# Kernel tuning notes

Measured on AMD Instinct MI355X. Metric: run time of the kernel, lower is better.

The kernel has to match this reference:

```python
import jax, jax.numpy as jnp
import numpy as np

N, NF, DIM, H, DH, DEPTH, EDIM, NB = 256, 127, 128, 8, 64, 6, 3, 512
INNER = H * DH  # 512
SCALE = DH ** -0.5
EPS = 1e-5


def setup_inputs() -> dict:
    key = jax.random.key(0)
    ks = jax.random.split(key, 16)
    p = lambda k, shape: jax.random.normal(k, shape, jnp.float32) * 0.02
    return {
        "coordinates": jax.random.normal(ks[0], (N, 3), jnp.float32),
        "bonds": jax.random.randint(ks[1], (NB, 2), 0, N),
        "noise_level": jax.random.uniform(ks[2], (1,), jnp.float32),
        "atom_emb": p(ks[3], (N, NF)),
        "ln1_g": jnp.ones((DEPTH, DIM)), "ln1_b": jnp.zeros((DEPTH, DIM)),
        "Wq": p(ks[4], (DEPTH, DIM, INNER)), "bq": jnp.zeros((DEPTH, INNER)),
        "Wkv": p(ks[5], (DEPTH, DIM, 2 * INNER)), "bkv": jnp.zeros((DEPTH, 2 * INNER)),
        "We": p(ks[6], (DEPTH, EDIM, INNER)), "be": jnp.zeros((DEPTH, INNER)),
        "Wo": p(ks[7], (DEPTH, INNER, DIM)), "bo": jnp.zeros((DEPTH, DIM)),
        "Wg1": p(ks[8], (DEPTH, 3 * DIM)),
        "ln2_g": jnp.ones((DEPTH, DIM)), "ln2_b": jnp.zeros((DEPTH, DIM)),
        "W1": p(ks[9], (DEPTH, DIM, 4 * DIM)), "b1": jnp.zeros((DEPTH, 4 * DIM)),
        "W2": p(ks[10], (DEPTH, 4 * DIM, DIM)), "b2": jnp.zeros((DEPTH, DIM)),
        "Wg2": p(ks[11], (DEPTH, 3 * DIM)),
        "out_w": p(ks[12], (DIM, 1)), "out_b": jnp.zeros((1,)),
    }


def _layernorm(x, g, b):
    m = jnp.mean(x, axis=-1, keepdims=True)
    v = jnp.mean((x - m) ** 2, axis=-1, keepdims=True)
    return (x - m) * jax.lax.rsqrt(v + EPS) * g + b


def _gated_residual(x, res, Wg):
    # Linear(3*dim -> 1, no bias) then sigmoid; mask is all-True so no masking.
    gate = jax.nn.sigmoid(jnp.concatenate([x, res, x - res], axis=-1) @ Wg)[..., None]
    return x * gate + res * (1.0 - gate)


def _forward(coordinates, bonds, noise_level, atom_emb, ln1_g, ln1_b, Wq, bq,
             Wkv, bkv, We, be, Wo, bo, Wg1, ln2_g, ln2_b, W1, b1, W2, b2, Wg2,
             out_w, out_b):
    n = coordinates.shape[0]
    # nodes: [n, NF] atom embeddings (looked up at arange(n)) + noise column -> [n, DIM]
    noise_col = jnp.broadcast_to(noise_level.reshape(1, 1), (n, 1))
    nodes = jnp.concatenate([atom_emb, noise_col], axis=-1)
    # dense edge tensor [n, n, 3]: coordinate differences at bonded pairs, antisymmetric
    bi, bj = bonds[:, 0], bonds[:, 1]
    diff = coordinates[bi] - coordinates[bj]
    edges = jnp.zeros((n, n, EDIM), jnp.float32).at[bi, bj].set(diff).at[bj, bi].set(-diff)

    for l in range(DEPTH):
        # --- edge-biased multi-head attention (PreNorm) ---
        x = _layernorm(nodes, ln1_g[l], ln1_b[l])
        q = (x @ Wq[l] + bq[l]).reshape(n, H, DH).transpose(1, 0, 2)          # [h, i, d]
        kv = x @ Wkv[l] + bkv[l]
        k = kv[:, :INNER].reshape(n, H, DH).transpose(1, 0, 2)                # [h, j, d]
        v = kv[:, INNER:].reshape(n, H, DH).transpose(1, 0, 2)                # [h, j, d]
        e = (edges @ We[l] + be[l]).reshape(n, n, H, DH).transpose(2, 0, 1, 3)  # [h, i, j, d]
        k_ij = k[:, None, :, :] + e                                            # [h, i, j, d]
        v_ij = v[:, None, :, :] + e
        sim = jnp.einsum('hid,hijd->hij', q, k_ij) * SCALE
        attn = jax.nn.softmax(sim, axis=-1)  # mask is all ones -> no-op
        out = jnp.einsum('hij,hijd->hid', attn, v_ij)                          # [h, i, d]
        out = out.transpose(1, 0, 2).reshape(n, INNER) @ Wo[l] + bo[l]         # [n, DIM]
        nodes = _gated_residual(out, nodes, Wg1[l])
        # --- feedforward (PreNorm) + gated residual ---
        y = _layernorm(nodes, ln2_g[l], ln2_b[l])
        y = jax.nn.gelu(y @ W1[l] + b1[l], approximate=False) @ W2[l] + b2[l]
        nodes = _gated_residual(y, nodes, Wg2[l])

    energy = nodes @ out_w + out_b  # [n, 1]
    return energy[None, :, :]       # [1, n, 1]


def reference(coordinates, bonds, noise_level, atom_emb, ln1_g, ln1_b, Wq, bq,
              Wkv, bkv, We, be, Wo, bo, Wg1, ln2_g, ln2_b, W1, b1, W2, b2, Wg2,
              out_w, out_b):
    return _forward(coordinates, bonds, noise_level, atom_emb, ln1_g, ln1_b,
                    Wq, bq, Wkv, bkv, We, be, Wo, bo, Wg1, ln2_g, ln2_b,
                    W1, b1, W2, b2, Wg2, out_w, out_b)
```

## Files before the change

### kernel.cpp

```cpp
#include <hip/hip_runtime.h>

#define NN     256
#define NF     127
#define DIM    128
#define NH     8
#define DH     64
#define INNER  512
#define DEPTH  6
#define NB     512
#define ATTN_SCALE 0.125f
#define LN_EPS 1e-5f

#define FMA4(A_, S_, V_) { A_.x=fmaf(S_,(V_).x,A_.x); A_.y=fmaf(S_,(V_).y,A_.y); \
                           A_.z=fmaf(S_,(V_).z,A_.z); A_.w=fmaf(S_,(V_).w,A_.w); }

__device__ __forceinline__ float wred_sum(float v){
#pragma unroll
  for(int o=32;o;o>>=1) v += __shfl_xor(v,o);
  return v;
}
__device__ __forceinline__ float wred_max(float v){
#pragma unroll
  for(int o=32;o;o>>=1) v = fmaxf(v,__shfl_xor(v,o));
  return v;
}
__device__ __forceinline__ float2 wred_sum2(float a, float b){
#pragma unroll
  for(int o=32;o;o>>=1){ a += __shfl_xor(a,o); b += __shfl_xor(b,o); }
  return make_float2(a,b);
}

__device__ __forceinline__ void ln_wave(float n0, float n1,
                                        const float* g, const float* b, int l,
                                        float& x0, float& x1){
  float2 sv = wred_sum2(n0+n1, n0*n0+n1*n1);
  float m  = sv.x*(1.f/DIM);
  float var = sv.y*(1.f/DIM) - m*m;
  float rs = rsqrtf(var + LN_EPS);
  x0 = (n0-m)*rs*g[l]    + b[l];
  x1 = (n1-m)*rs*g[64+l] + b[64+l];
}

__device__ __forceinline__ void gate_wave(float o0, float o1, float& n0, float& n1,
                                          const float* Wg, int l){
  float gv = o0*Wg[l]    + n0*Wg[DIM+l]    + (o0-n0)*Wg[2*DIM+l]
           + o1*Wg[64+l] + n1*Wg[DIM+64+l] + (o1-n1)*Wg[2*DIM+64+l];
  gv = wred_sum(gv);
  float gate = 1.f/(1.f + expf(-gv));
  n0 = o0*gate + n0*(1.f-gate);
  n1 = o1*gate + n1*(1.f-gate);
}

__device__ __forceinline__ void mvp128_512(const float* xin, const float* W,
                                           float* SC, int t){
  const int cg4 = (t&127)<<2, fq = t>>7;
  float4 acc = make_float4(0.f,0.f,0.f,0.f);
#pragma unroll 8
  for(int f=fq*32; f<fq*32+32; f++){
    float4 wv = *(const float4*)(W + f*INNER + cg4);
    float xv = xin[f];
    FMA4(acc, xv, wv);
  }
  *(float4*)(SC + fq*INNER + cg4) = acc;
}
__device__ __forceinline__ void mvp128_1024(const float* xin, const float* W,
                                            float* SC, int t){
  const int cg4 = (t&255)<<2, rh = t>>8;
  float4 acc = make_float4(0.f,0.f,0.f,0.f);
#pragma unroll 8
  for(int f=rh*64; f<rh*64+64; f++){
    float4 wv = *(const float4*)(W + f*(2*INNER) + cg4);
    float xv = xin[f];
    FMA4(acc, xv, wv);
  }
  *(float4*)(SC + rh*(2*INNER) + cg4) = acc;
}
__device__ __forceinline__ void mvp512_128(const float* ain, const float* W,
                                           float* SC, int t){
  const int cg4 = (t&31)<<2, fg = t>>5;
  float4 acc = make_float4(0.f,0.f,0.f,0.f);
#pragma unroll 8
  for(int f=fg*32; f<fg*32+32; f++){
    float4 wv = *(const float4*)(W + f*DIM + cg4);
    float av = ain[f];
    FMA4(acc, av, wv);
  }
  *(float4*)(SC + fg*DIM + cg4) = acc;
}

__device__ __forceinline__ void qkv_tail(const float* xs, int i,
    const float* Wq, const float* bq, const float* Wkv, const float* bkv,
    const float* be, float* qgn, float* kTn, float* vgn, float* SC, int t){
  mvp128_512(xs, Wq, SC, t);
  __syncthreads();
  qgn[i*INNER + t] = bq[t] + SC[t] + SC[INNER+t] + SC[2*INNER+t] + SC[3*INNER+t];
  __syncthreads();
  mvp128_1024(xs, Wkv, SC, t);
  __syncthreads();
#pragma unroll
  for(int cc=0; cc<2; cc++){
    int c = t + cc*512;
    float s = bkv[c] + SC[c] + SC[2*INNER+c];
    if(c < INNER) kTn[c*NN + i]            = s + be[c];
    else          vgn[i*INNER + c - INNER] = s + be[c-INNER];
  }
}

__global__ __launch_bounds__(512) void k_qkv0(const float* atom_emb, const float* noise,
    float* nodes, const float* ln1_g, const float* ln1_b,
    const float* Wq, const float* bq, const float* Wkv, const float* bkv, const float* be,
    float* qg, float* kT, float* vg,
    const int* bonds, const float* coords, float* ebg){
  __shared__ __align__(16) float SC[2048];
  __shared__ __align__(16) float xsm[DIM];
  __shared__ __align__(16) float ebs[8*768];
  const int t = threadIdx.x, bid = blockIdx.x;
  if(bid >= NN){
    const int i0 = (bid-NN)<<3;
#pragma unroll
    for(int cc=0; cc<12; cc++) ebs[cc*512 + t] = 0.f;
    __syncthreads();
    {
      const int bi = bonds[2*t], bj = bonds[2*t+1];
      const bool hi = (bi>=i0 && bi<i0+8), hj = (bj>=i0 && bj<i0+8);
      if(hi || hj){
        float dx = coords[3*bi+0] - coords[3*bj+0];
        float dy = coords[3*bi+1] - coords[3*bj+1];
        float dz = coords[3*bi+2] - coords[3*bj+2];
        if(hi){ float* e = ebs + (bi-i0)*768; e[bj]=dx;  e[256+bj]=dy;  e[512+bj]=dz;  }
        if(hj){ float* e = ebs + (bj-i0)*768; e[bi]=-dx; e[256+bi]=-dy; e[512+bi]=-dz; }
      }
    }
    __syncthreads();
#pragma unroll
    for(int cc=0; cc<12; cc++) ebg[(size_t)i0*768 + cc*512 + t] = ebs[cc*512 + t];
    return;
  }
  const int i = bid, w = t>>6, l = t&63;
  float nd0 = (l<NF)?    atom_emb[i*NF + l]      : noise[0];
  float nd1 = (64+l<NF)? atom_emb[i*NF + 64 + l] : noise[0];
  if(w==0){ nodes[i*DIM + l] = nd0; nodes[i*DIM + 64 + l] = nd1; }
  float x0, x1;
  ln_wave(nd0, nd1, ln1_g, ln1_b, l, x0, x1);
  xsm[l] = x0; xsm[64+l] = x1;
  __syncthreads();
  qkv_tail(xsm, i, Wq, bq, Wkv, bkv, be, qg, kT, vg, SC, t);
}

__global__ __launch_bounds__(512) void k_attn(
    const float* __restrict__ qg, const float* __restrict__ kT,
    const float* __restrict__ vg, const float* __restrict__ ebg,
    const float* __restrict__ We, float* __restrict__ aog,
    const float* __restrict__ pfA, const float* __restrict__ pfB,
    const float* __restrict__ pfC, const float* __restrict__ pfD,
    const float* __restrict__ pfE, int pf_next)
{
  __shared__ __align__(16) float qsm[8*DH];
  __shared__ __align__(16) float aW[8][NN];
  const int t = threadIdx.x;
  const int h = blockIdx.x >> 5, i0 = (blockIdx.x & 31) << 3;
  const int w = t>>6, l = t&63;
  const int qb = h*DH, j0 = l<<2;

  qsm[w*DH + l] = qg[(i0+w)*INNER + qb + l];

  {
    const int s = blockIdx.x >> 3;
    float keep = 0.f;
    { float4 v = ((const float4*)pfA)[s*512 + t];  keep += v.x+v.y+v.z+v.w; }
    { float4 v = ((const float4*)pfB)[s*512 + t];  keep += v.x+v.y+v.z+v.w; }
    { float4 v = ((const float4*)pfC)[s*512 + t];  keep += v.x+v.y+v.z+v.w; }
    if(pf_next){
      { float4 v = ((const float4*)pfD)[s*512 + t];        keep += v.x+v.y+v.z+v.w; }
      { float4 v = ((const float4*)pfE)[s*1024 + t];       keep += v.x+v.y+v.z+v.w; }
      { float4 v = ((const float4*)pfE)[s*1024 + 512 + t]; keep += v.x+v.y+v.z+v.w; }
    }
    asm volatile("" :: "v"(keep));
  }
  __syncthreads();

  float qwe0, qwe1, qwe2;
  {
    float qv = qsm[w*DH + l];
    qwe0 = qv*We[0*INNER + qb + l];
    qwe1 = qv*We[1*INNER + qb + l];
    qwe2 = qv*We[2*INNER + qb + l];
#pragma unroll
    for(int o=32;o;o>>=1){
      qwe0 += __shfl_xor(qwe0,o); qwe1 += __shfl_xor(qwe1,o); qwe2 += __shfl_xor(qwe2,o);
    }
  }
  const float* __restrict__ kTh = kT + qb*NN;
  float s0=0.f,s1=0.f,s2=0.f,s3=0.f;
#pragma unroll 8
  for(int o=0;o<DH;o++){
    float qv = qsm[w*DH + o];
    float4 kk = *(const float4*)(kTh + o*NN + j0);
    s0=fmaf(qv,kk.x,s0); s1=fmaf(qv,kk.y,s1); s2=fmaf(qv,kk.z,s2); s3=fmaf(qv,kk.w,s3);
  }
  const float* __restrict__ e = ebg + (size_t)(i0+w)*768;
  float4 ex = *(const float4*)(e + j0);
  float4 ey = *(const float4*)(e + 256 + j0);
  float4 ez = *(const float4*)(e + 512 + j0);
  s0 = (s0 + qwe0*ex.x + qwe1*ey.x + qwe2*ez.x)*ATTN_SCALE;
  s1 = (s1 + qwe0*ex.y + qwe1*ey.y + qwe2*ez.y)*ATTN_SCALE;
  s2 = (s2 + qwe0*ex.z + qwe1*ey.z + qwe2*ez.z)*ATTN_SCALE;
  s3 = (s3 + qwe0*ex.w + qwe1*ey.w + qwe2*ez.w)*ATTN_SCALE;
  float mx = wred_max(fmaxf(fmaxf(s0,s1),fmaxf(s2,s3)));
  float p0=expf(s0-mx), p1=expf(s1-mx), p2=expf(s2-mx), p3=expf(s3-mx);
  float inv = 1.f / wred_sum(p0+p1+p2+p3);
  float a0=p0*inv, a1=p1*inv, a2=p2*inv, a3=p3*inv;
  *(float4*)(aW[w] + j0) = make_float4(a0,a1,a2,a3);
  float c0 = a0*ex.x + a1*ex.y + a2*ex.z + a3*ex.w;
  float c1 = a0*ey.x + a1*ey.y + a2*ey.z + a3*ey.w;
  float c2 = a0*ez.x + a1*ez.y + a2*ez.z + a3*ez.w;
  c0 = wred_sum(c0); c1 = wred_sum(c1); c2 = wred_sum(c2);
  __builtin_amdgcn_wave_barrier();
  const int dq = (l&15)<<2, jg = l>>4;
  const float* __restrict__ vb = vg + qb + dq;
  float4 acc = make_float4(0.f,0.f,0.f,0.f);
#pragma unroll 8
  for(int jj=0;jj<64;jj++){
    int j = (jg<<6) + ((jj + (jg<<3)) & 63);
    float a = aW[w][j];
    float4 vv = *(const float4*)(vb + j*INNER);
    FMA4(acc, a, vv);
  }
#pragma unroll
  for(int o=16;o<64;o<<=1){
    acc.x += __shfl_xor(acc.x,o); acc.y += __shfl_xor(acc.y,o);
    acc.z += __shfl_xor(acc.z,o); acc.w += __shfl_xor(acc.w,o);
  }
  if(l<16){
    float4 we0 = *(const float4*)(We + 0*INNER + qb + dq);
    float4 we1 = *(const float4*)(We + 1*INNER + qb + dq);
    float4 we2 = *(const float4*)(We + 2*INNER + qb + dq);
    float4 ov;
    ov.x = acc.x + c0*we0.x + c1*we1.x + c2*we2.x;
    ov.y = acc.y + c0*we0.y + c1*we1.y + c2*we2.y;
    ov.z = acc.z + c0*we0.z + c1*we1.z + c2*we2.z;
    ov.w = acc.w + c0*we0.w + c1*we1.w + c2*we2.w;
    *(float4*)(aog + (i0+w)*INNER + qb + dq) = ov;
  }
}

__global__ __launch_bounds__(512) void k_layer(
    float* nodes, const float* __restrict__ aog,
    float* qg_n, float* kT_n, float* vg_n,
    const float* __restrict__ Wo, const float* __restrict__ bo,
    const float* __restrict__ Wg1,
    const float* __restrict__ ln2_g, const float* __restrict__ ln2_b,
    const float* __restrict__ W1, const float* __restrict__ b1,
    const float* __restrict__ W2, const float* __restrict__ b2,
    const float* __restrict__ Wg2,
    const float* __restrict__ ln1_g_n, const float* __restrict__ ln1_b_n,
    const float* __restrict__ Wq_n, const float* __restrict__ bq_n,
    const float* __restrict__ Wkv_n, const float* __restrict__ bkv_n,
    const float* __restrict__ be_n,
    const float* __restrict__ out_w, const float* __restrict__ out_b,
    float* eout, int has_next)
{
  __shared__ __align__(16) float SC[2048];
  __shared__ __align__(16) float qs[INNER];
  __shared__ __align__(16) float aos[INNER];
  __shared__ __align__(16) float xsm[DIM];
  const int t = threadIdx.x, i = blockIdx.x;
  const int w = t>>6, l = t&63;

  aos[t] = aog[i*INNER + t];
  float nd0 = nodes[i*DIM + l];
  float nd1 = nodes[i*DIM + 64 + l];
  __syncthreads();

  mvp512_128(aos, Wo, SC, t);
  __syncthreads();
  {
    float o0 = bo[l], o1 = bo[64+l];
#pragma unroll
    for(int fg=0; fg<16; fg++){ o0 += SC[fg*DIM + l]; o1 += SC[fg*DIM + 64 + l]; }
    gate_wave(o0, o1, nd0, nd1, Wg1, l);
    float x0, x1;
    ln_wave(nd0, nd1, ln2_g, ln2_b, l, x0, x1);
    xsm[l] = x0; xsm[64+l] = x1;
  }
  __syncthreads();

  mvp128_512(xsm, W1, SC, t);
  __syncthreads();
  {
    float a = b1[t] + SC[t] + SC[INNER+t] + SC[2*INNER+t] + SC[3*INNER+t];
    qs[t] = 0.5f*a*(1.f + erff(a*0.70710678118654752440f));
  }
  __syncthreads();
  mvp512_128(qs, W2, SC, t);
  __syncthreads();
  {
    float y0 = b2[l], y1 = b2[64+l];
#pragma unroll
    for(int fg=0; fg<16; fg++){ y0 += SC[fg*DIM + l]; y1 += SC[fg*DIM + 64 + l]; }
    gate_wave(y0, y1, nd0, nd1, Wg2, l);
    if(w==0){ nodes[i*DIM + l] = nd0; nodes[i*DIM + 64 + l] = nd1; }
    if(has_next){
      float x0, x1;
      ln_wave(nd0, nd1, ln1_g_n, ln1_b_n, l, x0, x1);
      xsm[l] = x0; xsm[64+l] = x1;
    } else if(w==0){
      float ev = nd0*out_w[l] + nd1*out_w[64+l];
      ev = wred_sum(ev);
      if(l==0) eout[i] = ev + out_b[0];
    }
  }
  if(has_next){
    __syncthreads();
    qkv_tail(xsm, i, Wq_n, bq_n, Wkv_n, bkv_n, be_n,
             qg_n, kT_n, vg_n, SC, t);
  }
}

extern "C" void kernel_launch(void* const* d_in, const int* in_sizes, int n_in,
                              void* d_out, int out_size, void* d_ws, size_t ws_size,
                              hipStream_t stream){
  const float* coords   = (const float*)d_in[0];
  const int*   bonds    = (const int*  )d_in[1];
  const float* noise    = (const float*)d_in[2];
  const float* atom_emb = (const float*)d_in[3];
  const float* ln1_g = (const float*)d_in[4];
  const float* ln1_b = (const float*)d_in[5];
  const float* Wq    = (const float*)d_in[6];
  const float* bq    = (const float*)d_in[7];
  const float* Wkv   = (const float*)d_in[8];
  const float* bkv   = (const float*)d_in[9];
  const float* We    = (const float*)d_in[10];
  const float* be    = (const float*)d_in[11];
  const float* Wo    = (const float*)d_in[12];
  const float* bo    = (const float*)d_in[13];
  const float* Wg1   = (const float*)d_in[14];
  const float* ln2_g = (const float*)d_in[15];
  const float* ln2_b = (const float*)d_in[16];
  const float* W1    = (const float*)d_in[17];
  const float* b1    = (const float*)d_in[18];
  const float* W2    = (const float*)d_in[19];
  const float* b2    = (const float*)d_in[20];
  const float* Wg2   = (const float*)d_in[21];
  const float* out_w = (const float*)d_in[22];
  const float* out_b = (const float*)d_in[23];

  float* ws = (float*)d_ws;
  float* nodes   = ws;
  float* qbuf[2] = { ws +  32768, ws + 163840 };
  float* kbuf[2] = { ws + 294912, ws + 425984 };
  float* vbuf[2] = { ws + 557056, ws + 688128 };
  float* aobuf   = ws + 819200;
  float* ebg     = ws + 950272;

  k_qkv0<<<NN+32, 512, 0, stream>>>(atom_emb, noise, nodes, ln1_g, ln1_b,
                                    Wq, bq, Wkv, bkv, be,
                                    qbuf[0], kbuf[0], vbuf[0],
                                    bonds, coords, ebg);
  for(int l=0; l<DEPTH; l++){
    int cur = l&1, nxt = cur^1;
    int has_next = (l < DEPTH-1);
    int ln = has_next ? l+1 : l;
    const float* Wo_l = Wo + (size_t)l*INNER*DIM;
    const float* W1_l = W1 + (size_t)l*DIM*4*DIM;
    const float* W2_l = W2 + (size_t)l*4*DIM*DIM;
    const float* Wq_n = Wq  + (size_t)ln*DIM*INNER;
    const float* Wkv_n= Wkv + (size_t)ln*DIM*2*INNER;
    k_attn<<<NN, 512, 0, stream>>>(
      qbuf[cur], kbuf[cur], vbuf[cur], ebg,
      We + (size_t)l*3*INNER, aobuf,
      Wo_l, W1_l, W2_l, Wq_n, Wkv_n, has_next);
    k_layer<<<NN, 512, 0, stream>>>(
      nodes, aobuf,
      qbuf[nxt], kbuf[nxt], vbuf[nxt],
      Wo_l, bo + (size_t)l*DIM, Wg1 + (size_t)l*3*DIM,
      ln2_g + (size_t)l*DIM, ln2_b + (size_t)l*DIM,
      W1_l, b1 + (size_t)l*4*DIM,
      W2_l, b2 + (size_t)l*DIM, Wg2 + (size_t)l*3*DIM,
      ln1_g + (size_t)ln*DIM, ln1_b + (size_t)ln*DIM,
      Wq_n, bq + (size_t)ln*INNER,
      Wkv_n, bkv + (size_t)ln*2*INNER,
      be  + (size_t)ln*INNER,
      out_w, out_b, (float*)d_out, has_next);
  }
}
```

Before: 296.3 us.

## Convert Wq/Wo/W1/W2 weights to fp16 and overlap Q with KV matvec

Adds a prep kernel that converts the Wq, Wo, W1 and W2 weights to fp16 once per call. The per-node matrix-vector products then read half as many weight bytes, using 8-wide loads that accumulate in fp32. The L2 prefetch in the attention kernel is resized to match the fp16 layout. In qkv_tail, the Q and KV products now run back to back into separate shared-memory regions with a single barrier, which needs a larger shared buffer and adds an extra kernel launch plus fp16 rounding error in those weights.

```diff
diff --git a/kernel.cpp b/kernel.cpp
--- a/kernel.cpp
+++ b/kernel.cpp
@@ -11,6 +11,9 @@
 #define ATTN_SCALE 0.125f
 #define LN_EPS 1e-5f
 
+typedef _Float16 f16;
+union H8 { uint4 u; f16 h[8]; };
+
 #define FMA4(A_, S_, V_) { A_.x=fmaf(S_,(V_).x,A_.x); A_.y=fmaf(S_,(V_).y,A_.y); \
                            A_.z=fmaf(S_,(V_).z,A_.z); A_.w=fmaf(S_,(V_).w,A_.w); }
 
@@ -51,20 +54,45 @@
   n1 = o1*gate + n1*(1.f-gate);
 }
 
-__device__ __forceinline__ void mvp128_512(const float* xin, const float* W,
-                                           float* SC, int t){
-  const int cg4 = (t&127)<<2, fq = t>>7;
-  float4 acc = make_float4(0.f,0.f,0.f,0.f);
-#pragma unroll 8
-  for(int f=fq*32; f<fq*32+32; f++){
-    float4 wv = *(const float4*)(W + f*INNER + cg4);
-    float xv = xin[f];
-    FMA4(acc, xv, wv);
-  }
-  *(float4*)(SC + fq*INNER + cg4) = acc;
-}
-__device__ __forceinline__ void mvp128_1024(const float* xin, const float* W,
-                                            float* SC, int t){
+__device__ __forceinline__ void mvp128_512h(const float* __restrict__ xin,
+                                            const f16* __restrict__ W,
+                                            float* __restrict__ SC, int t){
+  const int cg8 = (t&63)<<3, fg = t>>6, f0 = fg<<4;
+  const f16* __restrict__ p = W + f0*INNER + cg8;
+  float4 a0 = make_float4(0.f,0.f,0.f,0.f), a1 = a0;
+#pragma unroll
+  for(int k=0;k<16;k++){
+    H8 wv; wv.u = *(const uint4*)(p + k*INNER);
+    float x = xin[f0+k];
+    a0.x=fmaf(x,(float)wv.h[0],a0.x); a0.y=fmaf(x,(float)wv.h[1],a0.y);
+    a0.z=fmaf(x,(float)wv.h[2],a0.z); a0.w=fmaf(x,(float)wv.h[3],a0.w);
+    a1.x=fmaf(x,(float)wv.h[4],a1.x); a1.y=fmaf(x,(float)wv.h[5],a1.y);
+    a1.z=fmaf(x,(float)wv.h[6],a1.z); a1.w=fmaf(x,(float)wv.h[7],a1.w);
+  }
+  *(float4*)(SC + fg*INNER + cg8)     = a0;
+  *(float4*)(SC + fg*INNER + cg8 + 4) = a1;
+}
+__device__ __forceinline__ void mvp512_128h(const float* __restrict__ ain,
+                                            const f16* __restrict__ W,
+                                            float* __restrict__ SC, int t){
+  const int cg8 = (t&15)<<3, fg = t>>4, f0 = fg<<4;
+  const f16* __restrict__ p = W + f0*DIM + cg8;
+  float4 a0 = make_float4(0.f,0.f,0.f,0.f), a1 = a0;
+#pragma unroll
+  for(int k=0;k<16;k++){
+    H8 wv; wv.u = *(const uint4*)(p + k*DIM);
+    float x = ain[f0+k];
+    a0.x=fmaf(x,(float)wv.h[0],a0.x); a0.y=fmaf(x,(float)wv.h[1],a0.y);
+    a0.z=fmaf(x,(float)wv.h[2],a0.z); a0.w=fmaf(x,(float)wv.h[3],a0.w);
+    a1.x=fmaf(x,(float)wv.h[4],a1.x); a1.y=fmaf(x,(float)wv.h[5],a1.y);
+    a1.z=fmaf(x,(float)wv.h[6],a1.z); a1.w=fmaf(x,(float)wv.h[7],a1.w);
+  }
+  *(float4*)(SC + fg*DIM + cg8)     = a0;
+  *(float4*)(SC + fg*DIM + cg8 + 4) = a1;
+}
+__device__ __forceinline__ void mvp128_1024(const float* __restrict__ xin,
+                                            const float* __restrict__ W,
+                                            float* __restrict__ SC, int t){
   const int cg4 = (t&255)<<2, rh = t>>8;
   float4 acc = make_float4(0.f,0.f,0.f,0.f);
 #pragma unroll 8
@@ -75,43 +103,53 @@
   }
   *(float4*)(SC + rh*(2*INNER) + cg4) = acc;
 }
-__device__ __forceinline__ void mvp512_128(const float* ain, const float* W,
-                                           float* SC, int t){
-  const int cg4 = (t&31)<<2, fg = t>>5;
-  float4 acc = make_float4(0.f,0.f,0.f,0.f);
-#pragma unroll 8
-  for(int f=fg*32; f<fg*32+32; f++){
-    float4 wv = *(const float4*)(W + f*DIM + cg4);
-    float av = ain[f];
-    FMA4(acc, av, wv);
-  }
-  *(float4*)(SC + fg*DIM + cg4) = acc;
-}
-
-__device__ __forceinline__ void qkv_tail(const float* xs, int i,
-    const float* Wq, const float* bq, const float* Wkv, const float* bkv,
-    const float* be, float* qgn, float* kTn, float* vgn, float* SC, int t){
-  mvp128_512(xs, Wq, SC, t);
-  __syncthreads();
-  qgn[i*INNER + t] = bq[t] + SC[t] + SC[INNER+t] + SC[2*INNER+t] + SC[3*INNER+t];
-  __syncthreads();
-  mvp128_1024(xs, Wkv, SC, t);
-  __syncthreads();
+
+__device__ __forceinline__ void qkv_tail(const float* __restrict__ xs, int i,
+    const f16* __restrict__ Wqh, const float* __restrict__ bq,
+    const float* __restrict__ Wkv, const float* __restrict__ bkv,
+    const float* __restrict__ be, float* qgn, float* kTn, float* vgn,
+    float* __restrict__ SC, int t){
+  mvp128_512h(xs, Wqh, SC,        t);
+  mvp128_1024(xs, Wkv, SC + 4096, t);
+  __syncthreads();
+  {
+    float s = bq[t];
+#pragma unroll
+    for(int fg=0; fg<8; fg++) s += SC[fg*INNER + t];
+    qgn[i*INNER + t] = s;
+  }
 #pragma unroll
   for(int cc=0; cc<2; cc++){
     int c = t + cc*512;
-    float s = bkv[c] + SC[c] + SC[2*INNER+c];
-    if(c < INNER) kTn[c*NN + i]            = s + be[c];
-    else          vgn[i*INNER + c - INNER] = s + be[c-INNER];
+    float sv = bkv[c] + SC[4096 + c] + SC[4096 + 1024 + c];
+    if(c < INNER) kTn[c*NN + i]            = sv + be[c];
+    else          vgn[i*INNER + c - INNER] = sv + be[c-INNER];
+  }
+}
+
+__global__ __launch_bounds__(512) void k_prep(
+    const float* __restrict__ Wq, const float* __restrict__ Wo,
+    const float* __restrict__ W1, const float* __restrict__ W2,
+    f16* Wqh, f16* Woh, f16* W1h, f16* W2h)
+{
+  const int NQ = DEPTH*DIM*INNER;
+  const int NTOT = 4*NQ;
+  for(int k = blockIdx.x*512 + threadIdx.x; k < NTOT; k += gridDim.x*512){
+    float v; f16* dst;
+    if(k < NQ)        { v = Wq[k];        dst = Wqh + k; }
+    else if(k < 2*NQ) { v = Wo[k-NQ];     dst = Woh + (k-NQ); }
+    else if(k < 3*NQ) { v = W1[k-2*NQ];   dst = W1h + (k-2*NQ); }
+    else              { v = W2[k-3*NQ];   dst = W2h + (k-3*NQ); }
+    *dst = (f16)v;
   }
 }
 
 __global__ __launch_bounds__(512) void k_qkv0(const float* atom_emb, const float* noise,
     float* nodes, const float* ln1_g, const float* ln1_b,
-    const float* Wq, const float* bq, const float* Wkv, const float* bkv, const float* be,
+    const f16* Wqh, const float* bq, const float* Wkv, const float* bkv, const float* be,
     float* qg, float* kT, float* vg,
     const int* bonds, const float* coords, float* ebg){
-  __shared__ __align__(16) float SC[2048];
+  __shared__ __align__(16) float SC[6144];
   __shared__ __align__(16) float xsm[DIM];
   __shared__ __align__(16) float ebs[8*768];
   const int t = threadIdx.x, bid = blockIdx.x;
@@ -144,15 +182,15 @@
   ln_wave(nd0, nd1, ln1_g, ln1_b, l, x0, x1);
   xsm[l] = x0; xsm[64+l] = x1;
   __syncthreads();
-  qkv_tail(xsm, i, Wq, bq, Wkv, bkv, be, qg, kT, vg, SC, t);
+  qkv_tail(xsm, i, Wqh, bq, Wkv, bkv, be, qg, kT, vg, SC, t);
 }
 
 __global__ __launch_bounds__(512) void k_attn(
     const float* __restrict__ qg, const float* __restrict__ kT,
     const float* __restrict__ vg, const float* __restrict__ ebg,
     const float* __restrict__ We, float* __restrict__ aog,
-    const float* __restrict__ pfA, const float* __restrict__ pfB,
-    const float* __restrict__ pfC, const float* __restrict__ pfD,
+    const f16* __restrict__ pfA, const f16* __restrict__ pfB,
+    const f16* __restrict__ pfC, const f16* __restrict__ pfD,
     const float* __restrict__ pfE, int pf_next)
 {
   __shared__ __align__(16) float qsm[8*DH];
@@ -166,14 +204,17 @@
 
   {
     const int s = blockIdx.x >> 3;
-    float keep = 0.f;
-    { float4 v = ((const float4*)pfA)[s*512 + t];  keep += v.x+v.y+v.z+v.w; }
-    { float4 v = ((const float4*)pfB)[s*512 + t];  keep += v.x+v.y+v.z+v.w; }
-    { float4 v = ((const float4*)pfC)[s*512 + t];  keep += v.x+v.y+v.z+v.w; }
+    unsigned keep = 0u;
+    if(t < 256){
+      keep ^= ((const uint4*)((const char*)pfA + (size_t)s*4096))[t].x;
+      keep ^= ((const uint4*)((const char*)pfB + (size_t)s*4096))[t].y;
+      keep ^= ((const uint4*)((const char*)pfC + (size_t)s*4096))[t].z;
+      if(pf_next)
+        keep ^= ((const uint4*)((const char*)pfD + (size_t)s*4096))[t].w;
+    }
     if(pf_next){
-      { float4 v = ((const float4*)pfD)[s*512 + t];        keep += v.x+v.y+v.z+v.w; }
-      { float4 v = ((const float4*)pfE)[s*1024 + t];       keep += v.x+v.y+v.z+v.w; }
-      { float4 v = ((const float4*)pfE)[s*1024 + 512 + t]; keep += v.x+v.y+v.z+v.w; }
+      keep ^= ((const uint4*)((const char*)pfE + (size_t)s*16384))[t].x;
+      keep ^= ((const uint4*)((const char*)pfE + (size_t)s*16384))[512 + t].x;
     }
     asm volatile("" :: "v"(keep));
   }
@@ -247,20 +288,20 @@
 __global__ __launch_bounds__(512) void k_layer(
     float* nodes, const float* __restrict__ aog,
     float* qg_n, float* kT_n, float* vg_n,
-    const float* __restrict__ Wo, const float* __restrict__ bo,
+    const f16* __restrict__ Woh, const float* __restrict__ bo,
     const float* __restrict__ Wg1,
     const float* __restrict__ ln2_g, const float* __restrict__ ln2_b,
-    const float* __restrict__ W1, const float* __restrict__ b1,
-    const float* __restrict__ W2, const float* __restrict__ b2,
+    const f16* __restrict__ W1h, const float* __restrict__ b1,
+    const f16* __restrict__ W2h, const float* __restrict__ b2,
     const float* __restrict__ Wg2,
     const float* __restrict__ ln1_g_n, const float* __restrict__ ln1_b_n,
-    const float* __restrict__ Wq_n, const float* __restrict__ bq_n,
+    const f16* __restrict__ Wqh_n, const float* __restrict__ bq_n,
     const float* __restrict__ Wkv_n, const float* __restrict__ bkv_n,
     const float* __restrict__ be_n,
     const float* __restrict__ out_w, const float* __restrict__ out_b,
     float* eout, int has_next)
 {
-  __shared__ __align__(16) float SC[2048];
+  __shared__ __align__(16) float SC[6144];
   __shared__ __align__(16) float qs[INNER];
   __shared__ __align__(16) float aos[INNER];
   __shared__ __align__(16) float xsm[DIM];
@@ -272,12 +313,12 @@
   float nd1 = nodes[i*DIM + 64 + l];
   __syncthreads();
 
-  mvp512_128(aos, Wo, SC, t);
+  mvp512_128h(aos, Woh, SC, t);
   __syncthreads();
   {
     float o0 = bo[l], o1 = bo[64+l];
 #pragma unroll
-    for(int fg=0; fg<16; fg++){ o0 += SC[fg*DIM + l]; o1 += SC[fg*DIM + 64 + l]; }
+    for(int fg=0; fg<32; fg++){ o0 += SC[fg*DIM + l]; o1 += SC[fg*DIM + 64 + l]; }
     gate_wave(o0, o1, nd0, nd1, Wg1, l);
     float x0, x1;
     ln_wave(nd0, nd1, ln2_g, ln2_b, l, x0, x1);
@@ -285,19 +326,21 @@
   }
   __syncthreads();
 
-  mvp128_512(xsm, W1, SC, t);
-  __syncthreads();
-  {
-    float a = b1[t] + SC[t] + SC[INNER+t] + SC[2*INNER+t] + SC[3*INNER+t];
+  mvp128_512h(xsm, W1h, SC, t);
+  __syncthreads();
+  {
+    float a = b1[t];
+#pragma unroll
+    for(int fg=0; fg<8; fg++) a += SC[fg*INNER + t];
     qs[t] = 0.5f*a*(1.f + erff(a*0.70710678118654752440f));
   }
   __syncthreads();
-  mvp512_128(qs, W2, SC, t);
+  mvp512_128h(qs, W2h, SC, t);
   __syncthreads();
   {
     float y0 = b2[l], y1 = b2[64+l];
 #pragma unroll
-    for(int fg=0; fg<16; fg++){ y0 += SC[fg*DIM + l]; y1 += SC[fg*DIM + 64 + l]; }
+    for(int fg=0; fg<32; fg++){ y0 += SC[fg*DIM + l]; y1 += SC[fg*DIM + 64 + l]; }
     gate_wave(y0, y1, nd0, nd1, Wg2, l);
     if(w==0){ nodes[i*DIM + l] = nd0; nodes[i*DIM + 64 + l] = nd1; }
     if(has_next){
@@ -312,7 +355,7 @@
   }
   if(has_next){
     __syncthreads();
-    qkv_tail(xsm, i, Wq_n, bq_n, Wkv_n, bkv_n, be_n,
+    qkv_tail(xsm, i, Wqh_n, bq_n, Wkv_n, bkv_n, be_n,
              qg_n, kT_n, vg_n, SC, t);
   }
 }
@@ -345,42 +388,52 @@
   const float* out_w = (const float*)d_in[22];
   const float* out_b = (const float*)d_in[23];
 
-  float* ws = (float*)d_ws;
-  float* nodes   = ws;
-  float* qbuf[2] = { ws +  32768, ws + 163840 };
-  float* kbuf[2] = { ws + 294912, ws + 425984 };
-  float* vbuf[2] = { ws + 557056, ws + 688128 };
-  float* aobuf   = ws + 819200;
-  float* ebg     = ws + 950272;
-
+  char* base = (char*)d_ws;
+  float* nodes = (float*)(base);
+  float* qb0   = (float*)(base + 131072);
+  float* qb1   = (float*)(base + 655360);
+  float* aog   = (float*)(base + 1179648);
+  float* ebg   = (float*)(base + 1703936);
+  float* kb0   = (float*)(base + 2490368);
+  float* kb1   = (float*)(base + 3014656);
+  float* vb0   = (float*)(base + 3538944);
+  float* vb1   = (float*)(base + 4063232);
+  f16*   Wqh   = (f16*  )(base + 4587520);
+  f16*   Woh   = (f16*  )(base + 5373952);
+  f16*   W1h   = (f16*  )(base + 6160384);
+  f16*   W2h   = (f16*  )(base + 6946816);
+  float* eout  = (float*)d_out;
+
+  k_prep<<<512, 512, 0, stream>>>(Wq, Wo, W1, W2, Wqh, Woh, W1h, W2h);
   k_qkv0<<<NN+32, 512, 0, stream>>>(atom_emb, noise, nodes, ln1_g, ln1_b,
-                                    Wq, bq, Wkv, bkv, be,
-                                    qbuf[0], kbuf[0], vbuf[0],
+                                    Wqh, bq, Wkv, bkv, be,
+                                    qb0, kb0, vb0,
                                     bonds, coords, ebg);
   for(int l=0; l<DEPTH; l++){
-    int cur = l&1, nxt = cur^1;
     int has_next = (l < DEPTH-1);
     int ln = has_next ? l+1 : l;
-    const float* Wo_l = Wo + (size_t)l*INNER*DIM;
-    const float* W1_l = W1 + (size_t)l*DIM*4*DIM;
-    const float* W2_l = W2 + (size_t)l*4*DIM*DIM;
-    const float* Wq_n = Wq  + (size_t)ln*DIM*INNER;
-    const float* Wkv_n= Wkv + (size_t)ln*DIM*2*INNER;
+    float* qcur = (l&1)? qb1:qb0;  float* kcur = (l&1)? kb1:kb0;  float* vcur = (l&1)? vb1:vb0;
+    float* qnxt = (l&1)? qb0:qb1;  float* knxt = (l&1)? kb0:kb1;  float* vnxt = (l&1)? vb0:vb1;
+    const f16* Woh_l  = Woh + (size_t)l*INNER*DIM;
+    const f16* W1h_l  = W1h + (size_t)l*DIM*4*DIM;
+    const f16* W2h_l  = W2h + (size_t)l*4*DIM*DIM;
+    const f16* Wqh_n  = Wqh + (size_t)ln*DIM*INNER;
+    const float* Wkv_n = Wkv + (size_t)ln*DIM*2*INNER;
     k_attn<<<NN, 512, 0, stream>>>(
-      qbuf[cur], kbuf[cur], vbuf[cur], ebg,
-      We + (size_t)l*3*INNER, aobuf,
-      Wo_l, W1_l, W2_l, Wq_n, Wkv_n, has_next);
+      qcur, kcur, vcur, ebg,
+      We + (size_t)l*3*INNER, aog,
+      Woh_l, W1h_l, W2h_l, Wqh_n, Wkv_n, has_next);
     k_layer<<<NN, 512, 0, stream>>>(
-      nodes, aobuf,
-      qbuf[nxt], kbuf[nxt], vbuf[nxt],
-      Wo_l, bo + (size_t)l*DIM, Wg1 + (size_t)l*3*DIM,
+      nodes, aog,
+      qnxt, knxt, vnxt,
+      Woh_l, bo + (size_t)l*DIM, Wg1 + (size_t)l*3*DIM,
       ln2_g + (size_t)l*DIM, ln2_b + (size_t)l*DIM,
-      W1_l, b1 + (size_t)l*4*DIM,
-      W2_l, b2 + (size_t)l*DIM, Wg2 + (size_t)l*3*DIM,
+      W1h_l, b1 + (size_t)l*4*DIM,
+      W2h_l, b2 + (size_t)l*DIM, Wg2 + (size_t)l*3*DIM,
       ln1_g + (size_t)ln*DIM, ln1_b + (size_t)ln*DIM,
-      Wq_n, bq + (size_t)ln*INNER,
+      Wqh_n, bq + (size_t)ln*INNER,
       Wkv_n, bkv + (size_t)ln*2*INNER,
       be  + (size_t)ln*INNER,
-      out_w, out_b, (float*)d_out, has_next);
-  }
-}
+      out_w, out_b, eout, has_next);
+  }
+}
```

After: 286.5 us. 1.03x faster.
